# Kernel tuning notes

Measured on AMD Instinct MI355X. Metric: run time of the kernel, lower is better.

The kernel has to match this reference:

```python
import jax, jax.numpy as jnp
import numpy as np

DEPTH = 4      # truncation depth of the signature
DIM = 8        # path channels
PATH_LEN = 16384
STREAM = True


def _restricted_exp(z, depth):
    # exp(z) in truncated tensor algebra: level k term = z^{\otimes k}/k!, flattened to [d**k]
    terms = [z]
    for k in range(2, depth + 1):
        terms.append((terms[-1][:, None] * z[None, :]).reshape(-1) / k)
    return tuple(terms)


def _chen_mult(a, b, depth):
    # Truncated tensor-algebra product (Chen's relation); a_0 = b_0 = 1 implicit.
    # c_k = a_k + b_k + sum_{i=1}^{k-1} a_i \otimes b_{k-i}
    c = []
    for k in range(depth):
        t = a[k] + b[k]
        for i in range(k):
            t = t + (a[i][:, None] * b[k - 1 - i][None, :]).reshape(-1)
        c.append(t)
    return tuple(c)


def setup_inputs() -> dict:
    key = jax.random.key(0)
    path = jax.random.normal(key, (PATH_LEN, DIM), dtype=jnp.float32)
    return {"path": path}


def reference(path):
    depth = DEPTH
    d = path.shape[-1]
    inc = path[1:] - path[:-1]                                # [N-1, d] increments
    exps = jax.vmap(lambda z: _restricted_exp(z, depth))(inc)  # tuple of [N-1, d**k]
    init = tuple(jnp.zeros((d ** (k + 1),), dtype=path.dtype) for k in range(depth))

    def step(carry, x):
        new = _chen_mult(carry, x, depth)
        return new, (new if STREAM else None)

    last, ys = jax.lax.scan(step, init, exps)
    if STREAM:
        # flatten: concat levels -> [N-1, d + d^2 + ... + d^depth]
        return jnp.concatenate([y for y in ys], axis=-1)
    return jnp.concatenate(last, axis=-1)
```

## Files before the change

kernel.cpp:

```cpp
#include <hip/hip_runtime.h>

#define NPATH 16384
#define DIM   8
#define NINC  (NPATH - 1)
#define SIG   4680
#define L1OFF 0
#define L2OFF 8
#define L3OFF 72
#define L4OFF 584
#define NCHUNK 256
#define CHUNK  64
#define NSUB  1024
#define SUB   16
#define SPC   4
#define NGRP  16
#define GSIZE 16
#define C6    0.16666666666666666f
#define LPAD  17


__device__ __forceinline__ void light_barrier() {
  asm volatile("s_waitcnt lgkmcnt(0)" ::: "memory");
  __builtin_amdgcn_s_barrier();
}

__device__ __forceinline__ void zero_state(float r4[16], float r3[2],
                                           float& a1i, float& a2v,
                                           float& a2s, float& a1s, float& a1t) {
#pragma unroll
  for (int l = 0; l < 16; ++l) r4[l] = 0.f;
  r3[0] = r3[1] = 0.f;
  a1i = a2v = a2s = a1s = a1t = 0.f;
}

__device__ __forceinline__ void store_sig_reg(float* __restrict__ dst,
                                              const float r4[16], const float r3[2],
                                              float a2s, float a1t, int t) {
  float4* d4 = (float4*)(dst + L4OFF + 16 * t);
  d4[0] = make_float4(r4[0], r4[1], r4[2], r4[3]);
  d4[1] = make_float4(r4[4], r4[5], r4[6], r4[7]);
  d4[2] = make_float4(r4[8], r4[9], r4[10], r4[11]);
  d4[3] = make_float4(r4[12], r4[13], r4[14], r4[15]);
  *(float2*)(dst + L3OFF + 2 * t) = make_float2(r3[0], r3[1]);
  if (t < 64) dst[L2OFF + t] = a2s;
  if (t < 8)  dst[L1OFF + t] = a1t;
}

__device__ __forceinline__ void load_state(const float* __restrict__ src,
                                           float r4[16], float r3[2],
                                           float& a1i, float& a2v,
                                           float& a2s, float& a1s, float& a1t, int t) {
  const float4* s4 = (const float4*)(src + L4OFF + 16 * t);
  float4 G0 = s4[0], G1 = s4[1], G2 = s4[2], G3 = s4[3];
  r4[0]=G0.x; r4[1]=G0.y; r4[2]=G0.z; r4[3]=G0.w;
  r4[4]=G1.x; r4[5]=G1.y; r4[6]=G1.z; r4[7]=G1.w;
  r4[8]=G2.x; r4[9]=G2.y; r4[10]=G2.z; r4[11]=G2.w;
  r4[12]=G3.x; r4[13]=G3.y; r4[14]=G3.z; r4[15]=G3.w;
  const float2 gr3 = *(const float2*)(src + L3OFF + 2 * t);
  r3[0] = gr3.x; r3[1] = gr3.y;
  a1i = src[L1OFF + (t >> 5)];
  a2v = src[L2OFF + (t >> 2)];
  a2s = a1s = a1t = 0.f;
  if (t < 64) { a2s = src[L2OFF + t]; a1s = src[L1OFF + (t >> 3)]; }
  if (t < 8)  { a1t = src[L1OFF + t]; }
}

struct ChenB {
  float4 B0, B1, B2, B3;
  float4 C0, C1, C2, C3;
  float4 D0, D1, D2, D3;
  float4 E0, E1;
  float2 b3c, b2jk, b1k;
  float  b2ij, b1j, b1i, b2t, b1j2, b1i2, b1t;
};

__device__ __forceinline__ void chen_load(const float* __restrict__ b, int t, ChenB& R) {
  const int i   = t >> 5;
  const int j   = (t >> 2) & 7;
  const int ij  = t >> 2;
  const int c0  = 2 * t;
  const int jk0 = c0 & 63;
  const int k0  = 2 * (t & 3);
  const int i2  = t >> 3;
  const int j2  = t & 7;
  const float4* bv = (const float4*)b;
  R.B0 = bv[146 + 4 * t]; R.B1 = bv[147 + 4 * t]; R.B2 = bv[148 + 4 * t]; R.B3 = bv[149 + 4 * t];
  R.C0 = bv[18 + 2 * jk0]; R.C1 = bv[19 + 2 * jk0]; R.C2 = bv[20 + 2 * jk0]; R.C3 = bv[21 + 2 * jk0];
  R.D0 = bv[2 + 2 * k0]; R.D1 = bv[3 + 2 * k0]; R.D2 = bv[4 + 2 * k0]; R.D3 = bv[5 + 2 * k0];
  R.E0 = bv[0]; R.E1 = bv[1];
  R.b3c  = *(const float2*)(b + L3OFF + c0);
  R.b2jk = *(const float2*)(b + L2OFF + jk0);
  R.b1k  = *(const float2*)(b + L1OFF + k0);
  R.b2ij = b[L2OFF + ij];
  R.b1j  = b[L1OFF + j];
  R.b1i  = b[L1OFF + i];
  R.b2t = 0.f; R.b1j2 = 0.f; R.b1i2 = 0.f; R.b1t = 0.f;
  if (t < 64) { R.b2t = b[L2OFF + t]; R.b1j2 = b[L1OFF + j2]; R.b1i2 = b[L1OFF + i2]; }
  if (t < 8)  { R.b1t = b[L1OFF + t]; }
}

__device__ __forceinline__ void chen_apply(float r4[16], float r3[2],
                                           float& a1i, float& a2v,
                                           float& a2s, float& a1s, float& a1t,
                                           const ChenB& R, int t) {
  const float b4r[16] = {R.B0.x,R.B0.y,R.B0.z,R.B0.w, R.B1.x,R.B1.y,R.B1.z,R.B1.w,
                         R.B2.x,R.B2.y,R.B2.z,R.B2.w, R.B3.x,R.B3.y,R.B3.z,R.B3.w};
  const float b3r[16] = {R.C0.x,R.C0.y,R.C0.z,R.C0.w, R.C1.x,R.C1.y,R.C1.z,R.C1.w,
                         R.C2.x,R.C2.y,R.C2.z,R.C2.w, R.C3.x,R.C3.y,R.C3.z,R.C3.w};
  const float b2r[16] = {R.D0.x,R.D0.y,R.D0.z,R.D0.w, R.D1.x,R.D1.y,R.D1.z,R.D1.w,
                         R.D2.x,R.D2.y,R.D2.z,R.D2.w, R.D3.x,R.D3.y,R.D3.z,R.D3.w};
  const float b1r[8]  = {R.E0.x,R.E0.y,R.E0.z,R.E0.w, R.E1.x,R.E1.y,R.E1.z,R.E1.w};
#pragma unroll
  for (int l = 0; l < 8; ++l) {
    r4[l]     += b4r[l]     + a1i * b3r[l]     + a2v * b2r[l]     + r3[0] * b1r[l];
    r4[8 + l] += b4r[8 + l] + a1i * b3r[8 + l] + a2v * b2r[8 + l] + r3[1] * b1r[l];
  }
  r3[0] += R.b3c.x + a1i * R.b2jk.x + a2v * R.b1k.x;
  r3[1] += R.b3c.y + a1i * R.b2jk.y + a2v * R.b1k.y;
  const float a1i_old = a1i;
  a2v += R.b2ij + a1i_old * R.b1j;
  if (t < 64) { a2s += R.b2t + a1s * R.b1j2; a1s += R.b1i2; }
  a1i = a1i_old + R.b1i;
  if (t < 8) a1t += R.b1t;
}

__device__ __forceinline__ void step_update(const float* zs,
                                            float r4[16], float r3[2],
                                            float& a1i, float& a2v,
                                            float& a2s, float& a1s, float& a1t, int t) {
  const int i  = t >> 5;
  const int j  = (t >> 2) & 7;
  const int k0 = 2 * (t & 3);
  const int i2 = t >> 3;
  const int j2 = t & 7;
  const float zi = zs[i];
  const float zj = zs[j];
  const float2 zk = *(const float2*)(zs + k0);
  const float4 za = *(const float4*)zs;
  const float4 zb = *(const float4*)(zs + 4);
  const float zn[8] = {za.x, za.y, za.z, za.w, zb.x, zb.y, zb.z, zb.w};
  const float a1zi4 = a1i + 0.25f * zi;
  const float zj6   = C6 * zj;
  const float T0 = r3[0] + a2v * (0.5f * zk.x) + a1zi4 * (zj6 * zk.x);
  const float T1 = r3[1] + a2v * (0.5f * zk.y) + a1zi4 * (zj6 * zk.y);
  const float U  = a2v + (0.5f * a1i + C6 * zi) * zj;
#pragma unroll
  for (int l = 0; l < 8; ++l) {
    r4[l]     += T0 * zn[l];
    r4[8 + l] += T1 * zn[l];
  }
  r3[0] += zk.x * U;
  r3[1] += zk.y * U;
  a2v += (a1i + 0.5f * zi) * zj;
  a1i += zi;
  if (t < 64) {
    const float zi2 = zs[i2], zj2v = zs[j2];
    a2s += (a1s + 0.5f * zi2) * zj2v;
    a1s += zi2;
  }
  if (t < 8) a1t += zs[t];
}

__global__ __launch_bounds__(256) void k_totals(const float* __restrict__ path,
                                                float* __restrict__ T64,
                                                float* __restrict__ snap) {
  __shared__ float zbuf[CHUNK][8];
  const int t = threadIdx.x;
  const int b = blockIdx.x;
  const int base = b * CHUNK;
  for (int u = t; u < CHUNK * 8; u += 256) {
    const int s = u >> 3, l = u & 7;
    const int rB = min(base + s + 1, NPATH - 1);
    zbuf[s][l] = path[rB * DIM + l] - path[(base + s) * DIM + l];
  }
  float r4[16], r3[2], a1i, a2v, a2s, a1s, a1t;
  zero_state(r4, r3, a1i, a2v, a2s, a1s, a1t);
  __syncthreads();
  for (int w = 0; w < SPC; ++w) {
    if (w > 0) store_sig_reg(snap + ((size_t)b * SPC + w) * SIG, r4, r3, a2s, a1t, t);
#pragma unroll
    for (int s2 = 0; s2 < SUB; ++s2)
      step_update(zbuf[SUB * w + s2], r4, r3, a1i, a2v, a2s, a1s, a1t, t);
  }
  store_sig_reg(T64 + (size_t)b * SIG, r4, r3, a2s, a1t, t);
}

__global__ __launch_bounds__(256) void k_scan(const float* __restrict__ in,
                                              float* __restrict__ prefout,
                                              float* __restrict__ totout,
                                              int count) {
  const int t = threadIdx.x;
  const size_t goff = (size_t)blockIdx.x * count;
  float r4[16], r3[2], a1i, a2v, a2s, a1s, a1t;
  zero_state(r4, r3, a1i, a2v, a2s, a1s, a1t);
  ChenB bA, bB;
  chen_load(in + goff * SIG, t, bA);
  for (int m = 0; m < count; m += 2) {
    if (m + 1 < count) chen_load(in + (goff + m + 1) * SIG, t, bB);
    store_sig_reg(prefout + (goff + m) * SIG, r4, r3, a2s, a1t, t);
    chen_apply(r4, r3, a1i, a2v, a2s, a1s, a1t, bA, t);
    if (m + 1 >= count) break;
    if (m + 2 < count) chen_load(in + (goff + m + 2) * SIG, t, bA);
    store_sig_reg(prefout + (goff + m + 1) * SIG, r4, r3, a2s, a1t, t);
    chen_apply(r4, r3, a1i, a2v, a2s, a1s, a1t, bB, t);
  }
  if (totout != nullptr) store_sig_reg(totout + (size_t)blockIdx.x * SIG, r4, r3, a2s, a1t, t);
}

__global__ __launch_bounds__(256) void k_out(const float* __restrict__ path,
                                             const float* __restrict__ pref,
                                             const float* __restrict__ GT,
                                             const float* __restrict__ snap,
                                             float* __restrict__ out) {
  __shared__ float zbuf[SUB][8];
  __shared__ __align__(16) float lbuf[2][256 * LPAD];
  const int t = threadIdx.x;
  const int sIdx = blockIdx.x;
  const int b = sIdx >> 2;
  const int g = b >> 4;
  const int base = sIdx * SUB;
  const int n = min(SUB, NINC - base);
  if (t < SUB * 8) {
    const int s = t >> 3, l = t & 7;
    const int rB = min(base + s + 1, NPATH - 1);
    zbuf[s][l] = path[rB * DIM + l] - path[(base + s) * DIM + l];
  }
  float r4[16], r3[2], a1i, a2v, a2s, a1s, a1t;
  zero_state(r4, r3, a1i, a2v, a2s, a1s, a1t);
  const int cnt = g + 1 + ((sIdx & 3) ? 1 : 0);
#define PADDR(m) ((m) < g ? GT + (size_t)(m) * SIG \
                          : ((m) == g ? pref + (size_t)b * SIG : snap + (size_t)sIdx * SIG))
  ChenB cA, cB;
  chen_load(PADDR(0), t, cA);
  for (int m = 0; m < cnt; m += 2) {
    if (m + 1 < cnt) chen_load(PADDR(m + 1), t, cB);
    chen_apply(r4, r3, a1i, a2v, a2s, a1s, a1t, cA, t);
    if (m + 1 >= cnt) break;
    if (m + 2 < cnt) chen_load(PADDR(m + 2), t, cA);
    chen_apply(r4, r3, a1i, a2v, a2s, a1s, a1t, cB, t);
  }
#undef PADDR
  __syncthreads();
  const int tp = t >> 2;
  const int rq = 4 * (t & 3);
#pragma unroll 4
  for (int s2 = 0; s2 < n; ++s2) {
    step_update(zbuf[s2], r4, r3, a1i, a2v, a2s, a1s, a1t, t);
    float* lb = lbuf[s2 & 1] + LPAD * t;
    *(float4*)(lb + 0)  = make_float4(r4[0], r4[1], r4[2], r4[3]);
    *(float4*)(lb + 4)  = make_float4(r4[4], r4[5], r4[6], r4[7]);
    *(float4*)(lb + 8)  = make_float4(r4[8], r4[9], r4[10], r4[11]);
    *(float4*)(lb + 12) = make_float4(r4[12], r4[13], r4[14], r4[15]);
    light_barrier();
    const float* lbr = lbuf[s2 & 1];
    float* dst = out + (size_t)(base + s2) * SIG;
#pragma unroll
    for (int q = 0; q < 4; ++q) {
      const float4 v = *(const float4*)(lbr + LPAD * (tp + 64 * q) + rq);
      *(float4*)(dst + L4OFF + 4 * t + 1024 * q) = v;
    }
    *(float2*)(dst + L3OFF + 2 * t) = make_float2(r3[0], r3[1]);
    if (t < 64) dst[L2OFF + t] = a2s;
    if (t < 8)  dst[L1OFF + t] = a1t;
  }
}

extern "C" void kernel_launch(void* const* d_in, const int* in_sizes, int n_in,
                              void* d_out, int out_size, void* d_ws, size_t ws_size,
                              hipStream_t stream) {
  (void)in_sizes; (void)n_in; (void)out_size; (void)ws_size;
  const float* path = (const float*)d_in[0];
  float* out = (float*)d_out;
  float* ws = (float*)d_ws;

  float* T64    = ws;
  float* pref   = T64    + (size_t)NCHUNK * SIG;
  float* GT     = pref   + (size_t)NCHUNK * SIG;
  float* snap   = GT     + (size_t)NGRP * SIG;

  k_totals<<<NCHUNK, 256, 0, stream>>>(path, T64, snap);
  k_scan<<<NGRP, 256, 0, stream>>>(T64, pref, GT, GSIZE);
  k_out<<<NSUB, 256, 0, stream>>>(path, pref, GT, snap, out);
}
```

Measured before the change: 133.5 us.

## Split chunk totals into per-16-step sub-blocks plus a Chen fold kernel

Replaces the k_totals kernel, which ran 256 blocks over 64 sequential steps each. The new k_t16 kernel runs 1024 blocks over 16 steps each and writes sub-block signatures to a new T16 workspace. A new k_fold kernel then combines each group of four with Chen products to produce the snapshots and the 64-step totals. This exposes four times more parallelism in the first stage, which with 256 blocks may not have filled the GPU. The cost is an extra launch, a round trip of 1024 signatures through global memory, and three Chen products per chunk.

Measured after the change: 139.3 us. 4.4% more time.

```diff
diff --git a/kernel.cpp b/kernel.cpp
--- a/kernel.cpp
+++ b/kernel.cpp
@@ -161,27 +161,44 @@
   if (t < 8) a1t += zs[t];
 }
 
-__global__ __launch_bounds__(256) void k_totals(const float* __restrict__ path,
-                                                float* __restrict__ T64,
-                                                float* __restrict__ snap) {
-  __shared__ float zbuf[CHUNK][8];
+__global__ __launch_bounds__(256) void k_t16(const float* __restrict__ path,
+                                             float* __restrict__ T16) {
+  __shared__ float zbuf[SUB][8];
   const int t = threadIdx.x;
-  const int b = blockIdx.x;
-  const int base = b * CHUNK;
-  for (int u = t; u < CHUNK * 8; u += 256) {
-    const int s = u >> 3, l = u & 7;
+  const int sIdx = blockIdx.x;
+  const int base = sIdx * SUB;
+  if (t < SUB * 8) {
+    const int s = t >> 3, l = t & 7;
     const int rB = min(base + s + 1, NPATH - 1);
     zbuf[s][l] = path[rB * DIM + l] - path[(base + s) * DIM + l];
   }
   float r4[16], r3[2], a1i, a2v, a2s, a1s, a1t;
   zero_state(r4, r3, a1i, a2v, a2s, a1s, a1t);
   __syncthreads();
-  for (int w = 0; w < SPC; ++w) {
-    if (w > 0) store_sig_reg(snap + ((size_t)b * SPC + w) * SIG, r4, r3, a2s, a1t, t);
-#pragma unroll
-    for (int s2 = 0; s2 < SUB; ++s2)
-      step_update(zbuf[SUB * w + s2], r4, r3, a1i, a2v, a2s, a1s, a1t, t);
-  }
+#pragma unroll
+  for (int s2 = 0; s2 < SUB; ++s2)
+    step_update(zbuf[s2], r4, r3, a1i, a2v, a2s, a1s, a1t, t);
+  store_sig_reg(T16 + (size_t)sIdx * SIG, r4, r3, a2s, a1t, t);
+}
+
+__global__ __launch_bounds__(256) void k_fold(const float* __restrict__ T16,
+                                              float* __restrict__ T64,
+                                              float* __restrict__ snap) {
+  const int t = threadIdx.x;
+  const int b = blockIdx.x;
+  const size_t s0 = (size_t)b * SPC;
+  float r4[16], r3[2], a1i, a2v, a2s, a1s, a1t;
+  load_state(T16 + s0 * SIG, r4, r3, a1i, a2v, a2s, a1s, a1t, t);
+  ChenB cA, cB;
+  chen_load(T16 + (s0 + 1) * SIG, t, cA);
+  store_sig_reg(snap + (s0 + 1) * SIG, r4, r3, a2s, a1t, t);
+  chen_load(T16 + (s0 + 2) * SIG, t, cB);
+  chen_apply(r4, r3, a1i, a2v, a2s, a1s, a1t, cA, t);
+  store_sig_reg(snap + (s0 + 2) * SIG, r4, r3, a2s, a1t, t);
+  chen_load(T16 + (s0 + 3) * SIG, t, cA);
+  chen_apply(r4, r3, a1i, a2v, a2s, a1s, a1t, cB, t);
+  store_sig_reg(snap + (s0 + 3) * SIG, r4, r3, a2s, a1t, t);
+  chen_apply(r4, r3, a1i, a2v, a2s, a1s, a1t, cA, t);
   store_sig_reg(T64 + (size_t)b * SIG, r4, r3, a2s, a1t, t);
 }
 
@@ -277,8 +294,10 @@
   float* pref   = T64    + (size_t)NCHUNK * SIG;
   float* GT     = pref   + (size_t)NCHUNK * SIG;
   float* snap   = GT     + (size_t)NGRP * SIG;
-
-  k_totals<<<NCHUNK, 256, 0, stream>>>(path, T64, snap);
+  float* T16    = snap   + (size_t)NSUB * SIG;
+
+  k_t16<<<NSUB, 256, 0, stream>>>(path, T16);
+  k_fold<<<NCHUNK, 256, 0, stream>>>(T16, T64, snap);
   k_scan<<<NGRP, 256, 0, stream>>>(T64, pref, GT, GSIZE);
   k_out<<<NSUB, 256, 0, stream>>>(path, pref, GT, snap, out);
 }
```
